# Performance work log

Hardware: AMD Instinct MI355X
Metric: run time of the kernel (lower is better)

## Reference

```python
import jax, jax.numpy as jnp
import numpy as np

E, D, H, B, S = 16, 1024, 256, 4, 4096  # num_splats, model_dim, ff_dim//num_splats, batch, seq_len


def setup_inputs() -> dict:
    key = jax.random.key(0)
    ks = jax.random.split(key, 8)
    s = 0.02  # init scale for stability
    return {
        "x": jax.random.normal(ks[0], (B, S, D), dtype=jnp.float32),
        "splat_id": jax.random.randint(ks[1], (S,), 0, E, dtype=jnp.int32),
        "W1": jax.random.normal(ks[2], (E, D, H), dtype=jnp.float32) * s,
        "b1": jnp.zeros((E, H), dtype=jnp.float32),
        "W2": jax.random.normal(ks[3], (E, H, D), dtype=jnp.float32) * s,
        "b2": jnp.zeros((E, D), dtype=jnp.float32),
        "Wg1": jax.random.normal(ks[4], (D, D), dtype=jnp.float32) * s,
        "bg1": jnp.zeros((D,), dtype=jnp.float32),
        "Wg2": jax.random.normal(ks[5], (D, D), dtype=jnp.float32) * s,
        "bg2": jnp.zeros((D,), dtype=jnp.float32),
    }


def reference(x, splat_id, W1, b1, W2, b2, Wg1, bg1, Wg2, bg2):
    # Splat-aware dispatch: token s is processed by expert splat_id[s].
    # Equivalent vectorized form: run every expert's small MLP, mask at the
    # hidden layer by expert assignment, and sum over experts (each token is
    # assigned to exactly one expert, matching the gather->MLP->scatter loop).
    nE = W1.shape[0]
    onehot = (splat_id[None, :] == jnp.arange(nE, dtype=splat_id.dtype)[:, None]).astype(x.dtype)  # [E,S]
    # hidden: [E,B,S,H]
    h = jax.nn.gelu(jnp.einsum('bsd,edh->ebsh', x, W1) + b1[:, None, None, :], approximate=False)
    h = h * onehot[:, None, :, None]  # zero tokens not routed to expert e
    routed = jnp.einsum('ebsh,ehd->bsd', h, W2)  # [B,S,D]
    routed = routed + jnp.einsum('es,ed->sd', onehot, b2)[None, :, :]  # per-token expert bias
    # global aggregator MLP (torch GELU default = exact erf form)
    g = jax.nn.gelu(routed @ Wg1 + bg1, approximate=False)
    return g @ Wg2 + bg2
```

## Files before the change

kernel.cpp:

```cpp
#include <hip/hip_runtime.h>


#define DEV __device__ __forceinline__

typedef float f32x4 __attribute__((ext_vector_type(4)));
typedef float f32x16 __attribute__((ext_vector_type(16)));
typedef short short8 __attribute__((ext_vector_type(8)));

DEV unsigned short f2bf(float f) {
  unsigned u = __float_as_uint(f);
  u += 0x7fffu + ((u >> 16) & 1u);
  return (unsigned short)(u >> 16);
}

DEV void gload_lds16(const void* g, void* l) {
  __builtin_amdgcn_global_load_lds(
      (const __attribute__((address_space(1))) unsigned int*)g,
      (__attribute__((address_space(3))) unsigned int*)l, 16, 0, 0);
}

DEV float gelu_exact(float v) {
  return 0.5f * v * (1.0f + erff(v * 0.70710678118654752f));
}

#define BARRIER() __builtin_amdgcn_s_barrier()
#define VMW(n)    asm volatile("s_waitcnt vmcnt(" #n ")" ::: "memory")

__global__ __launch_bounds__(256) void prep_kernel(
    const float* __restrict__ x, unsigned short* __restrict__ xb,
    const float* __restrict__ W1, unsigned short* __restrict__ w1t,
    const float* __restrict__ W2, unsigned short* __restrict__ w2t,
    const float* __restrict__ Wg1, unsigned short* __restrict__ wg1t,
    const float* __restrict__ Wg2, unsigned short* __restrict__ wg2t) {
  __shared__ float tile[64][65];
  const int t = threadIdx.x;
  int id = (int)blockIdx.x;
  if (id < 8192) {
    long i = ((long)id * 256 + t) * 8;
    float4 v0 = *(const float4*)(x + i);
    float4 v1 = *(const float4*)(x + i + 4);
    uint4 o;
    o.x = (unsigned)f2bf(v0.x) | ((unsigned)f2bf(v0.y) << 16);
    o.y = (unsigned)f2bf(v0.z) | ((unsigned)f2bf(v0.w) << 16);
    o.z = (unsigned)f2bf(v1.x) | ((unsigned)f2bf(v1.y) << 16);
    o.w = (unsigned)f2bf(v1.z) | ((unsigned)f2bf(v1.w) << 16);
    *(uint4*)(xb + i) = o;
    return;
  }
  id -= 8192;
  const float* in; unsigned short* out;
  int R, C, r0, c0; long base;
  if (id < 1024) {
    in = W1; out = w1t; R = 1024; C = 256;
    base = (long)(id >> 6) * 262144;
    r0 = ((id >> 2) & 15) * 64; c0 = (id & 3) * 64;
  } else if (id < 2048) {
    id -= 1024;
    in = W2; out = w2t; R = 256; C = 1024;
    base = (long)(id >> 6) * 262144;
    r0 = ((id >> 4) & 3) * 64; c0 = (id & 15) * 64;
  } else if (id < 2304) {
    id -= 2048;
    in = Wg1; out = wg1t; R = 1024; C = 1024; base = 0;
    r0 = (id >> 4) * 64; c0 = (id & 15) * 64;
  } else {
    id -= 2304;
    in = Wg2; out = wg2t; R = 1024; C = 1024; base = 0;
    r0 = (id >> 4) * 64; c0 = (id & 15) * 64;
  }
  const int cc = t & 63, rr = t >> 6;
#pragma unroll
  for (int i = 0; i < 16; i++) {
    int r = rr + i * 4;
    tile[r][cc] = in[base + (long)(r0 + r) * C + (c0 + cc)];
  }
  __syncthreads();
#pragma unroll
  for (int i = 0; i < 16; i++) {
    int c = rr + i * 4;
    out[base + (long)(c0 + c) * R + (r0 + cc)] = f2bf(tile[cc][c]);
  }
}

__global__ __launch_bounds__(256) void route_kernel(
    const int* __restrict__ sid, int S, int* __restrict__ offs, int* __restrict__ order,
    int* __restrict__ tileE, int* __restrict__ tileR, int* __restrict__ ntl) {
  __shared__ int cnt[16], cur[16];
  const int t = threadIdx.x;
  if (t < 16) cnt[t] = 0;
  __syncthreads();
  for (int s = t; s < S; s += 256) atomicAdd(&cnt[sid[s]], 1);
  __syncthreads();
  if (t == 0) {
    int a = 0;
    for (int e = 0; e < 16; e++) { offs[e] = a; cur[e] = a; a += cnt[e]; }
    offs[16] = a;
    int nt = 0;
    for (int e = 0; e < 16; e++) {
      const int rows = 4 * cnt[e];
      for (int r = 0; r < rows; r += 128) {
        tileE[nt] = e;
        tileR[nt] = 4 * offs[e] + r;
        nt++;
      }
    }
    ntl[0] = nt;
  }
  __syncthreads();
  for (int s = t; s < S; s += 256) {
    int p = atomicAdd(&cur[sid[s]], 1);
    order[p] = s;
  }
}

template <bool GATHER_A, bool SCATTER_C, bool GELU, bool OUT_F32>
__global__ __launch_bounds__(256) void gemm_mfma(
    const unsigned short* __restrict__ A, const unsigned short* __restrict__ BT,
    const float* __restrict__ bias, void* __restrict__ Cout,
    int N, int K,
    const int* __restrict__ order, const int* __restrict__ offs,
    const int* __restrict__ tileE, const int* __restrict__ tileR,
    const int* __restrict__ ntl,
    int S, long btStride, int biasStride) {
  const int ti = (int)blockIdx.y;
  if (ti >= ntl[0]) return;
  const int t = (int)threadIdx.x;
  const int lane = t & 63;
  const int w = t >> 6;
  const int wm = w >> 1, wn = w & 1;
  const int tileN = (int)blockIdx.x;

  const int e = tileE[ti];
  const int rowBase = tileR[ti];
  int Me = 4 * offs[e + 1] - rowBase;
  if (Me > 128) Me = 128;
  const unsigned short* bt = BT + (long)e * btStride;
  const float* bs = bias + (long)e * biasStride;

  __shared__ __align__(16) unsigned short lA[128 * 64];
  __shared__ __align__(16) unsigned short lB[128 * 64];

  const unsigned short* aSrc[4];
  const unsigned short* bSrc[4];
  {
    const int q = t & 7;
#pragma unroll
    for (int i = 0; i < 4; i++) {
      const int row = i * 32 + (t >> 3);
      const int koff = ((q * 16) ^ ((row & 7) << 4)) >> 1;
      const int rr = (row < Me) ? row : (Me - 1);
      const int g = rowBase + rr;
      long arow;
      if (GATHER_A) {
        const int s = order[g >> 2];
        arow = (long)(g & 3) * S + s;
      } else {
        arow = g;
      }
      aSrc[i] = A + arow * (long)K + koff;
      const int col = tileN * 128 + row;
      bSrc[i] = bt + (long)col * K + koff;
    }
  }

  f32x4 acc[4][4] = {};

  const int KT = K >> 6;
  for (int kt = 0; kt < KT; kt++) {
    __syncthreads();
#pragma unroll
    for (int i = 0; i < 4; i++) {
      gload_lds16(aSrc[i] + (kt << 6), (void*)(lA + i * 2048 + w * 512));
      gload_lds16(bSrc[i] + (kt << 6), (void*)(lB + i * 2048 + w * 512));
    }
    __syncthreads();
#pragma unroll
    for (int kk = 0; kk < 2; kk++) {
      short8 af[4], bfr[4];
      const int kbyte = kk * 64 + (lane >> 4) * 16;
#pragma unroll
      for (int mi = 0; mi < 4; mi++) {
        const int row = wm * 64 + mi * 16 + (lane & 15);
        const int off = row * 128 + (kbyte ^ ((row & 7) << 4));
        af[mi] = *(const short8*)((const char*)lA + off);
      }
#pragma unroll
      for (int ni = 0; ni < 4; ni++) {
        const int row = wn * 64 + ni * 16 + (lane & 15);
        const int off = row * 128 + (kbyte ^ ((row & 7) << 4));
        bfr[ni] = *(const short8*)((const char*)lB + off);
      }
#pragma unroll
      for (int mi = 0; mi < 4; mi++)
#pragma unroll
        for (int ni = 0; ni < 4; ni++)
          acc[mi][ni] = __builtin_amdgcn_mfma_f32_16x16x32_bf16(af[mi], bfr[ni], acc[mi][ni], 0, 0, 0);
    }
  }

  float bcol[4];
#pragma unroll
  for (int ni = 0; ni < 4; ni++)
    bcol[ni] = bs[tileN * 128 + wn * 64 + ni * 16 + (lane & 15)];

#pragma unroll
  for (int mi = 0; mi < 4; mi++) {
#pragma unroll
    for (int j = 0; j < 4; j++) {
      const int lrow = wm * 64 + mi * 16 + ((lane >> 4) * 4) + j;
      if (lrow >= Me) continue;
      const int g = rowBase + lrow;
      long crow;
      if (SCATTER_C) crow = (long)(g & 3) * S + order[g >> 2];
      else crow = g;
#pragma unroll
      for (int ni = 0; ni < 4; ni++) {
        float v = acc[mi][ni][j] + bcol[ni];
        if (GELU) v = gelu_exact(v);
        const long cidx = crow * (long)N + tileN * 128 + wn * 64 + ni * 16 + (lane & 15);
        if (OUT_F32) ((float*)Cout)[cidx] = v;
        else ((unsigned short*)Cout)[cidx] = f2bf(v);
      }
    }
  }
}

template <bool GELU, bool OUT_F32>
__global__ __launch_bounds__(512, 2) void gemm_8p32(
    const unsigned short* __restrict__ A, const unsigned short* __restrict__ BT,
    const float* __restrict__ bias, void* __restrict__ Cout,
    int N, int K, int ntiles) {
  __shared__ __align__(16) unsigned short lds[8 * 8192];

  const int t = (int)threadIdx.x;
  const int lane = t & 63;
  const int w = t >> 6;
  const int wm = w >> 2;
  const int wn = w & 3;

  const int cpx = (int)gridDim.x >> 3;
  const int swz = ((int)blockIdx.x & 7) * cpx + ((int)blockIdx.x >> 3);
  const int mtile = swz / ntiles, ntile = swz % ntiles;

  const int tq = t & 7;
  const unsigned short* srcA[2][2];
  const unsigned short* srcB[2][2];
#pragma unroll
  for (int i = 0; i < 2; i++) {
    const int ir = i * 64 + (t >> 3);
    const int koffE = ((tq * 16) ^ ((ir & 7) << 4)) >> 1;
#pragma unroll
    for (int h = 0; h < 2; h++) {
      const int ra = (ir & 63) + (h << 6) + ((ir >> 6) << 7);
      srcA[i][h] = A + (long)(mtile * 256 + ra) * K + koffE;
      const int cb = (ir & 31) + (h << 5) + ((ir >> 5) << 6);
      srcB[i][h] = BT + (long)(ntile * 256 + cb) * K + koffE;
    }
  }
  const int dstE = (t >> 3) * 64 + tq * 8;

  auto STAGE = [&](int d, int mat, int h, int kt) {
    unsigned short* dst = lds + ((d * 4 + mat * 2 + h) << 13) + dstE;
    const unsigned short* s0 = (mat == 0 ? srcA[0][h] : srcB[0][h]) + (kt << 6);
    const unsigned short* s1 = (mat == 0 ? srcA[1][h] : srcB[1][h]) + (kt << 6);
    gload_lds16(s0, dst);
    gload_lds16(s1, dst + 4096);
  };

  short8 aR[2][4], bR[2][4];
  const int kcol = ((lane >> 5) << 4);
  const int l31 = lane & 31;

  auto LDA = [&](int d, int mh) {
    const char* base = (const char*)(lds + ((d * 4 + mh) << 13));
    const int r0 = wm * 64 + l31;
#pragma unroll
    for (int m = 0; m < 2; m++) {
      const int row = r0 + m * 32;
      const int rs = (row & 7) << 4;
#pragma unroll
      for (int kk = 0; kk < 4; kk++)
        aR[m][kk] = *(const short8*)(base + row * 128 + ((kk * 32 + kcol) ^ rs));
    }
  };
  auto LDB = [&](int d, int nh) {
    const char* base = (const char*)(lds + ((d * 4 + 2 + nh) << 13));
    const int col = wn * 32 + l31;
    const int rs = (col & 7) << 4;
#pragma unroll
    for (int kk = 0; kk < 4; kk++)
      bR[nh][kk] = *(const short8*)(base + col * 128 + ((kk * 32 + kcol) ^ rs));
  };

  f32x16 acc[4][2] = {};
  auto MMA = [&](int mh, int nh) {
    __builtin_amdgcn_s_setprio(1);
#pragma unroll
    for (int kk = 0; kk < 4; kk++)
#pragma unroll
      for (int m = 0; m < 2; m++)
        acc[mh * 2 + m][nh] = __builtin_amdgcn_mfma_f32_32x32x16_bf16(
            aR[m][kk], bR[nh][kk], acc[mh * 2 + m][nh], 0, 0, 0);
    __builtin_amdgcn_s_setprio(0);
  };

  const int KT = K >> 6;

  {
    const int t1 = (KT > 1) ? 1 : 0;
    STAGE(0, 0, 0, 0); STAGE(0, 1, 0, 0); STAGE(0, 1, 1, 0); STAGE(0, 0, 1, 0);
    STAGE(1, 0, 0, t1); STAGE(1, 1, 0, t1); STAGE(1, 1, 1, t1);
    VMW(6);
    BARRIER();
  }

  for (int it = 0; it < (KT >> 1); ++it) {
    const int tb = (2 * it + 1 < KT) ? 2 * it + 1 : KT - 1;
    int nx = 2 * it + 2; if (nx >= KT) nx = KT - 1;
    int ny = 2 * it + 3; if (ny >= KT) ny = KT - 1;
    LDA(0, 0); LDB(0, 0); STAGE(1, 0, 1, tb);
    BARRIER();
    MMA(0, 0);
    BARRIER();
    LDB(0, 1); STAGE(0, 0, 0, nx);
    BARRIER();
    MMA(0, 1);
    BARRIER();
    LDA(0, 1); STAGE(0, 1, 0, nx);
    BARRIER();
    MMA(1, 0);
    BARRIER();
    STAGE(0, 1, 1, nx);
    BARRIER();
    MMA(1, 1);
    VMW(6);
    BARRIER();
    LDA(1, 0); LDB(1, 0); STAGE(0, 0, 1, nx);
    BARRIER();
    MMA(0, 0);
    BARRIER();
    LDB(1, 1); STAGE(1, 0, 0, ny);
    BARRIER();
    MMA(0, 1);
    BARRIER();
    LDA(1, 1); STAGE(1, 1, 0, ny);
    BARRIER();
    MMA(1, 0);
    BARRIER();
    STAGE(1, 1, 1, ny);
    BARRIER();
    MMA(1, 1);
    VMW(6);
    BARRIER();
  }
  VMW(0);

  float bc[2];
#pragma unroll
  for (int n = 0; n < 2; n++)
    bc[n] = bias[ntile * 256 + wn * 64 + n * 32 + l31];
  const int cbase = ntile * 256 + wn * 64 + l31;
  const int rbase = mtile * 256 + wm * 128 + ((lane >> 5) << 2);
#pragma unroll
  for (int mf = 0; mf < 4; mf++) {
#pragma unroll
    for (int reg = 0; reg < 16; reg++) {
      const long crow = rbase + mf * 32 + (reg & 3) + ((reg >> 2) << 3);
#pragma unroll
      for (int nf = 0; nf < 2; nf++) {
        float v = acc[mf][nf][reg] + bc[nf];
        if (GELU) v = gelu_exact(v);
        const long cidx = crow * (long)N + cbase + nf * 32;
        if (OUT_F32) ((float*)Cout)[cidx] = v;
        else ((unsigned short*)Cout)[cidx] = f2bf(v);
      }
    }
  }
}

extern "C" void kernel_launch(void* const* d_in, const int* in_sizes, int n_in,
                              void* d_out, int out_size, void* d_ws, size_t ws_size,
                              hipStream_t stream) {
  const float* x   = (const float*)d_in[0];
  const int*   sid = (const int*)d_in[1];
  const float* W1  = (const float*)d_in[2];
  const float* b1  = (const float*)d_in[3];
  const float* W2  = (const float*)d_in[4];
  const float* b2  = (const float*)d_in[5];
  const float* Wg1 = (const float*)d_in[6];
  const float* bg1 = (const float*)d_in[7];
  const float* Wg2 = (const float*)d_in[8];
  const float* bg2 = (const float*)d_in[9];
  (void)in_sizes; (void)n_in; (void)out_size; (void)ws_size;

  constexpr int D = 1024, H = 256, S = 4096, B = 4;
  constexpr long NT = (long)B * S;

  char* ws = (char*)d_ws;
  unsigned short* xb   = (unsigned short*)(ws);
  unsigned short* w1t  = (unsigned short*)(ws + 33554432);
  unsigned short* w2t  = (unsigned short*)(ws + 41943040);
  unsigned short* wg1t = (unsigned short*)(ws + 50331648);
  unsigned short* wg2t = (unsigned short*)(ws + 52428800);
  unsigned short* hbuf = (unsigned short*)(ws + 54525952);
  unsigned short* rout = (unsigned short*)(ws + 62914560);
  int* offs  = (int*)(ws + 96468992);
  int* order = (int*)(ws + 96469248);
  int* tileE = (int*)(ws + 96485632);
  int* tileR = (int*)(ws + 96486208);
  int* ntl   = (int*)(ws + 96486784);

  prep_kernel<<<dim3(10752), 256, 0, stream>>>(x, xb, W1, w1t, W2, w2t, Wg1, wg1t, Wg2, wg2t);
  route_kernel<<<1, 256, 0, stream>>>(sid, S, offs, order, tileE, tileR, ntl);

  gemm_mfma<true, false, true, false><<<dim3(H / 128, 144), 256, 0, stream>>>(
      xb, w1t, b1, hbuf, H, D, order, offs, tileE, tileR, ntl, S, (long)H * D, H);
  gemm_mfma<false, true, false, false><<<dim3(D / 128, 144), 256, 0, stream>>>(
      hbuf, w2t, b2, rout, D, H, order, offs, tileE, tileR, ntl, S, (long)D * H, D);
  gemm_8p32<true, false><<<dim3((unsigned)(NT / 256) * (D / 256)), 512, 0, stream>>>(
      rout, wg1t, bg1, xb, D, D, D / 256);
  gemm_8p32<false, true><<<dim3((unsigned)(NT / 256) * (D / 256)), 512, 0, stream>>>(
      xb, wg2t, bg2, d_out, D, D, D / 256);
}
```

Before: 194.6 us.

## Use 2-phase double-buffered GEMM for Wg1 and 16x16 MFMA in 8-phase kernel

Adds a new simple double-buffered GEMM (one stage load then a full 64-wide K compute per iteration, 16x16x32 MFMA, one block per CU) used for the first aggregator GEMM. The existing 8-phase kernel, kept for the second GEMM, is converted from 32x32x16 to 16x16x32 MFMA with a matching fragment layout and epilogue. The aim is to change the instruction mix and the synchronisation pattern of the aggregator GEMMs. The simpler kernel uses fewer barriers but gives up some load/compute overlap and occupancy.

```diff
diff --git a/kernel.cpp b/kernel.cpp
--- a/kernel.cpp
+++ b/kernel.cpp
@@ -4,7 +4,6 @@
 #define DEV __device__ __forceinline__
 
 typedef float f32x4 __attribute__((ext_vector_type(4)));
-typedef float f32x16 __attribute__((ext_vector_type(16)));
 typedef short short8 __attribute__((ext_vector_type(8)));
 
 DEV unsigned short f2bf(float f) {
@@ -13,7 +12,7 @@
   return (unsigned short)(u >> 16);
 }
 
-DEV void gload_lds16(const void* g, void* l) {
+DEV void gload16(const void* g, void* l) {
   __builtin_amdgcn_global_load_lds(
       (const __attribute__((address_space(1))) unsigned int*)g,
       (__attribute__((address_space(3))) unsigned int*)l, 16, 0, 0);
@@ -170,8 +169,8 @@
     __syncthreads();
 #pragma unroll
     for (int i = 0; i < 4; i++) {
-      gload_lds16(aSrc[i] + (kt << 6), (void*)(lA + i * 2048 + w * 512));
-      gload_lds16(bSrc[i] + (kt << 6), (void*)(lB + i * 2048 + w * 512));
+      gload16(aSrc[i] + (kt << 6), (void*)(lA + i * 2048 + w * 512));
+      gload16(bSrc[i] + (kt << 6), (void*)(lB + i * 2048 + w * 512));
     }
     __syncthreads();
 #pragma unroll
@@ -226,11 +225,11 @@
 }
 
 template <bool GELU, bool OUT_F32>
-__global__ __launch_bounds__(512, 2) void gemm_8p32(
+__global__ __launch_bounds__(512, 1) void gemm_2ph(
     const unsigned short* __restrict__ A, const unsigned short* __restrict__ BT,
     const float* __restrict__ bias, void* __restrict__ Cout,
     int N, int K, int ntiles) {
-  __shared__ __align__(16) unsigned short lds[8 * 8192];
+  __shared__ __align__(16) unsigned short lds[2][2][256 * 64];
 
   const int t = (int)threadIdx.x;
   const int lane = t & 63;
@@ -243,6 +242,100 @@
   const int mtile = swz / ntiles, ntile = swz % ntiles;
 
   const int tq = t & 7;
+  const unsigned short* srcA[4];
+  const unsigned short* srcB[4];
+#pragma unroll
+  for (int i = 0; i < 4; i++) {
+    const int row = i * 64 + (t >> 3);
+    const int koffE = ((tq * 16) ^ ((row & 7) << 4)) >> 1;
+    srcA[i] = A + (long)(mtile * 256 + row) * K + koffE;
+    srcB[i] = BT + (long)(ntile * 256 + row) * K + koffE;
+  }
+  const int dstE = (t >> 3) * 64 + tq * 8;
+
+  auto STAGE = [&](int buf, int kt) {
+    const long ko = (long)kt << 6;
+#pragma unroll
+    for (int i = 0; i < 4; i++) gload16(srcA[i] + ko, &lds[buf][0][i * 4096 + dstE]);
+#pragma unroll
+    for (int i = 0; i < 4; i++) gload16(srcB[i] + ko, &lds[buf][1][i * 4096 + dstE]);
+  };
+
+  f32x4 acc[8][4] = {};
+  const int KT = K >> 6;
+
+  STAGE(0, 0);
+  __syncthreads();
+
+  int buf = 0;
+  for (int kt = 0; kt < KT; kt++) {
+    if (kt + 1 < KT) STAGE(buf ^ 1, kt + 1);
+#pragma unroll
+    for (int kk = 0; kk < 2; kk++) {
+      short8 aF[8], bF[4];
+      const int kb = kk * 64 + ((lane >> 4) << 4);
+#pragma unroll
+      for (int m = 0; m < 8; m++) {
+        const int row = wm * 128 + m * 16 + (lane & 15);
+        aF[m] = *(const short8*)((const char*)&lds[buf][0][0] + row * 128 + (kb ^ ((row & 7) << 4)));
+      }
+#pragma unroll
+      for (int n = 0; n < 4; n++) {
+        const int row = wn * 64 + n * 16 + (lane & 15);
+        bF[n] = *(const short8*)((const char*)&lds[buf][1][0] + row * 128 + (kb ^ ((row & 7) << 4)));
+      }
+      __builtin_amdgcn_s_setprio(1);
+#pragma unroll
+      for (int m = 0; m < 8; m++)
+#pragma unroll
+        for (int n = 0; n < 4; n++)
+          acc[m][n] = __builtin_amdgcn_mfma_f32_16x16x32_bf16(aF[m], bF[n], acc[m][n], 0, 0, 0);
+      __builtin_amdgcn_s_setprio(0);
+    }
+    __syncthreads();
+    buf ^= 1;
+  }
+
+  float bcol[4];
+#pragma unroll
+  for (int n = 0; n < 4; n++)
+    bcol[n] = bias[ntile * 256 + wn * 64 + n * 16 + (lane & 15)];
+  const int cbase = ntile * 256 + wn * 64 + (lane & 15);
+#pragma unroll
+  for (int m = 0; m < 8; m++) {
+#pragma unroll
+    for (int j = 0; j < 4; j++) {
+      const long crow = mtile * 256 + wm * 128 + m * 16 + ((lane >> 4) << 2) + j;
+#pragma unroll
+      for (int n = 0; n < 4; n++) {
+        float v = acc[m][n][j] + bcol[n];
+        if (GELU) v = gelu_exact(v);
+        const long cidx = crow * (long)N + cbase + n * 16;
+        if (OUT_F32) ((float*)Cout)[cidx] = v;
+        else ((unsigned short*)Cout)[cidx] = f2bf(v);
+      }
+    }
+  }
+}
+
+template <bool GELU, bool OUT_F32>
+__global__ __launch_bounds__(512, 2) void gemm_8phase(
+    const unsigned short* __restrict__ A, const unsigned short* __restrict__ BT,
+    const float* __restrict__ bias, void* __restrict__ Cout,
+    int N, int K, int ntiles) {
+  __shared__ __align__(16) unsigned short lds[8 * 8192];
+
+  const int t = (int)threadIdx.x;
+  const int lane = t & 63;
+  const int w = t >> 6;
+  const int wm = w >> 2;
+  const int wn = w & 3;
+
+  const int cpx = (int)gridDim.x >> 3;
+  const int swz = ((int)blockIdx.x & 7) * cpx + ((int)blockIdx.x >> 3);
+  const int mtile = swz / ntiles, ntile = swz % ntiles;
+
+  const int tq = t & 7;
   const unsigned short* srcA[2][2];
   const unsigned short* srcB[2][2];
 #pragma unroll
@@ -263,44 +356,48 @@
     unsigned short* dst = lds + ((d * 4 + mat * 2 + h) << 13) + dstE;
     const unsigned short* s0 = (mat == 0 ? srcA[0][h] : srcB[0][h]) + (kt << 6);
     const unsigned short* s1 = (mat == 0 ? srcA[1][h] : srcB[1][h]) + (kt << 6);
-    gload_lds16(s0, dst);
-    gload_lds16(s1, dst + 4096);
+    gload16(s0, dst);
+    gload16(s1, dst + 4096);
   };
 
-  short8 aR[2][4], bR[2][4];
-  const int kcol = ((lane >> 5) << 4);
-  const int l31 = lane & 31;
+  short8 aReg[8], bReg[8];
+  const int klane = (lane >> 4) << 4;
+  const int rsw = (lane & 7) << 4;
 
   auto LDA = [&](int d, int mh) {
     const char* base = (const char*)(lds + ((d * 4 + mh) << 13));
-    const int r0 = wm * 64 + l31;
-#pragma unroll
-    for (int m = 0; m < 2; m++) {
-      const int row = r0 + m * 32;
-      const int rs = (row & 7) << 4;
-#pragma unroll
-      for (int kk = 0; kk < 4; kk++)
-        aR[m][kk] = *(const short8*)(base + row * 128 + ((kk * 32 + kcol) ^ rs));
+    const int r0 = wm * 64 + (lane & 15);
+#pragma unroll
+    for (int m = 0; m < 4; m++) {
+      const int row = r0 + m * 16;
+#pragma unroll
+      for (int kk = 0; kk < 2; kk++)
+        aReg[m * 2 + kk] = *(const short8*)(base + row * 128 + ((kk * 64 + klane) ^ rsw));
     }
   };
   auto LDB = [&](int d, int nh) {
     const char* base = (const char*)(lds + ((d * 4 + 2 + nh) << 13));
-    const int col = wn * 32 + l31;
-    const int rs = (col & 7) << 4;
-#pragma unroll
-    for (int kk = 0; kk < 4; kk++)
-      bR[nh][kk] = *(const short8*)(base + col * 128 + ((kk * 32 + kcol) ^ rs));
+    const int r0 = wn * 32 + (lane & 15);
+#pragma unroll
+    for (int n = 0; n < 2; n++) {
+      const int row = r0 + n * 16;
+#pragma unroll
+      for (int kk = 0; kk < 2; kk++)
+        bReg[(nh * 2 + n) * 2 + kk] = *(const short8*)(base + row * 128 + ((kk * 64 + klane) ^ rsw));
+    }
   };
 
-  f32x16 acc[4][2] = {};
-  auto MMA = [&](int mh, int nh) {
+  f32x4 acc[8][4] = {};
+  auto MMA = [&](int mb, int nb) {
     __builtin_amdgcn_s_setprio(1);
 #pragma unroll
-    for (int kk = 0; kk < 4; kk++)
-#pragma unroll
-      for (int m = 0; m < 2; m++)
-        acc[mh * 2 + m][nh] = __builtin_amdgcn_mfma_f32_32x32x16_bf16(
-            aR[m][kk], bR[nh][kk], acc[mh * 2 + m][nh], 0, 0, 0);
+    for (int kk = 0; kk < 2; kk++)
+#pragma unroll
+      for (int m = 0; m < 4; m++)
+#pragma unroll
+        for (int n = 0; n < 2; n++)
+          acc[mb + m][nb + n] = __builtin_amdgcn_mfma_f32_16x16x32_bf16(
+              aReg[m * 2 + kk], bReg[(nb + n) * 2 + kk], acc[mb + m][nb + n], 0, 0, 0);
     __builtin_amdgcn_s_setprio(0);
   };
 
@@ -324,15 +421,15 @@
     BARRIER();
     LDB(0, 1); STAGE(0, 0, 0, nx);
     BARRIER();
-    MMA(0, 1);
+    MMA(0, 2);
     BARRIER();
     LDA(0, 1); STAGE(0, 1, 0, nx);
     BARRIER();
-    MMA(1, 0);
+    MMA(4, 0);
     BARRIER();
     STAGE(0, 1, 1, nx);
     BARRIER();
-    MMA(1, 1);
+    MMA(4, 2);
     VMW(6);
     BARRIER();
     LDA(1, 0); LDB(1, 0); STAGE(0, 0, 1, nx);
@@ -341,36 +438,35 @@
     BARRIER();
     LDB(1, 1); STAGE(1, 0, 0, ny);
     BARRIER();
-    MMA(0, 1);
+    MMA(0, 2);
     BARRIER();
     LDA(1, 1); STAGE(1, 1, 0, ny);
     BARRIER();
-    MMA(1, 0);
+    MMA(4, 0);
     BARRIER();
     STAGE(1, 1, 1, ny);
     BARRIER();
-    MMA(1, 1);
+    MMA(4, 2);
     VMW(6);
     BARRIER();
   }
   VMW(0);
 
-  float bc[2];
-#pragma unroll
-  for (int n = 0; n < 2; n++)
-    bc[n] = bias[ntile * 256 + wn * 64 + n * 32 + l31];
-  const int cbase = ntile * 256 + wn * 64 + l31;
-  const int rbase = mtile * 256 + wm * 128 + ((lane >> 5) << 2);
-#pragma unroll
-  for (int mf = 0; mf < 4; mf++) {
-#pragma unroll
-    for (int reg = 0; reg < 16; reg++) {
-      const long crow = rbase + mf * 32 + (reg & 3) + ((reg >> 2) << 3);
-#pragma unroll
-      for (int nf = 0; nf < 2; nf++) {
-        float v = acc[mf][nf][reg] + bc[nf];
+  float bcol[4];
+#pragma unroll
+  for (int n = 0; n < 4; n++)
+    bcol[n] = bias[ntile * 256 + wn * 64 + n * 16 + (lane & 15)];
+  const int cbase = ntile * 256 + wn * 64 + (lane & 15);
+#pragma unroll
+  for (int m = 0; m < 8; m++) {
+#pragma unroll
+    for (int j = 0; j < 4; j++) {
+      const long crow = mtile * 256 + wm * 128 + m * 16 + ((lane >> 4) << 2) + j;
+#pragma unroll
+      for (int n = 0; n < 4; n++) {
+        float v = acc[m][n][j] + bcol[n];
         if (GELU) v = gelu_exact(v);
-        const long cidx = crow * (long)N + cbase + nf * 32;
+        const long cidx = crow * (long)N + cbase + n * 16;
         if (OUT_F32) ((float*)Cout)[cidx] = v;
         else ((unsigned short*)Cout)[cidx] = f2bf(v);
       }
@@ -417,8 +513,8 @@
       xb, w1t, b1, hbuf, H, D, order, offs, tileE, tileR, ntl, S, (long)H * D, H);
   gemm_mfma<false, true, false, false><<<dim3(D / 128, 144), 256, 0, stream>>>(
       hbuf, w2t, b2, rout, D, H, order, offs, tileE, tileR, ntl, S, (long)D * H, D);
-  gemm_8p32<true, false><<<dim3((unsigned)(NT / 256) * (D / 256)), 512, 0, stream>>>(
+  gemm_2ph<true, false><<<dim3((unsigned)(NT / 256) * (D / 256)), 512, 0, stream>>>(
       rout, wg1t, bg1, xb, D, D, D / 256);
-  gemm_8p32<false, true><<<dim3((unsigned)(NT / 256) * (D / 256)), 512, 0, stream>>>(
+  gemm_8phase<false, true><<<dim3((unsigned)(NT / 256) * (D / 256)), 512, 0, stream>>>(
       xb, wg2t, bg2, d_out, D, D, D / 256);
 }
```

Measured after the change: 186.5 us. 1.04x faster.

## Replace 256x256 ping-pong dense GEMM with simple 128x128 tile kernel

Applied to the files above, without the earlier changes.

The aggregator GEMMs move from a 512-thread, 256x256-tile kernel with a hand-scheduled double-buffered LDS pipeline and 32x32 MFMAs to a 256-thread, 128x128-tile kernel. The new kernel uses a single LDS buffer with two syncthreads per k-step and 16x16x32 MFMAs, the same scheme as the routed GEMM. This gives four times as many blocks and more occupancy per CU, but loses the overlap of loads with MFMA and the higher arithmetic intensity of the larger tiles.

```diff
diff --git a/kernel.cpp b/kernel.cpp
--- a/kernel.cpp
+++ b/kernel.cpp
@@ -4,7 +4,6 @@
 #define DEV __device__ __forceinline__
 
 typedef float f32x4 __attribute__((ext_vector_type(4)));
-typedef float f32x16 __attribute__((ext_vector_type(16)));
 typedef short short8 __attribute__((ext_vector_type(8)));
 
 DEV unsigned short f2bf(float f) {
@@ -13,7 +12,7 @@
   return (unsigned short)(u >> 16);
 }
 
-DEV void gload_lds16(const void* g, void* l) {
+DEV void gload16(const void* g, void* l) {
   __builtin_amdgcn_global_load_lds(
       (const __attribute__((address_space(1))) unsigned int*)g,
       (__attribute__((address_space(3))) unsigned int*)l, 16, 0, 0);
@@ -22,9 +21,6 @@
 DEV float gelu_exact(float v) {
   return 0.5f * v * (1.0f + erff(v * 0.70710678118654752f));
 }
-
-#define BARRIER() __builtin_amdgcn_s_barrier()
-#define VMW(n)    asm volatile("s_waitcnt vmcnt(" #n ")" ::: "memory")
 
 __global__ __launch_bounds__(256) void prep_kernel(
     const float* __restrict__ x, unsigned short* __restrict__ xb,
@@ -170,8 +166,8 @@
     __syncthreads();
 #pragma unroll
     for (int i = 0; i < 4; i++) {
-      gload_lds16(aSrc[i] + (kt << 6), (void*)(lA + i * 2048 + w * 512));
-      gload_lds16(bSrc[i] + (kt << 6), (void*)(lB + i * 2048 + w * 512));
+      gload16(aSrc[i] + (kt << 6), (void*)(lA + i * 2048 + w * 512));
+      gload16(bSrc[i] + (kt << 6), (void*)(lB + i * 2048 + w * 512));
     }
     __syncthreads();
 #pragma unroll
@@ -226,151 +222,85 @@
 }
 
 template <bool GELU, bool OUT_F32>
-__global__ __launch_bounds__(512, 2) void gemm_8p32(
+__global__ __launch_bounds__(256, 4) void gemm_dense128(
     const unsigned short* __restrict__ A, const unsigned short* __restrict__ BT,
     const float* __restrict__ bias, void* __restrict__ Cout,
     int N, int K, int ntiles) {
-  __shared__ __align__(16) unsigned short lds[8 * 8192];
-
   const int t = (int)threadIdx.x;
   const int lane = t & 63;
   const int w = t >> 6;
-  const int wm = w >> 2;
-  const int wn = w & 3;
+  const int wm = w >> 1, wn = w & 1;
 
   const int cpx = (int)gridDim.x >> 3;
   const int swz = ((int)blockIdx.x & 7) * cpx + ((int)blockIdx.x >> 3);
   const int mtile = swz / ntiles, ntile = swz % ntiles;
 
-  const int tq = t & 7;
-  const unsigned short* srcA[2][2];
-  const unsigned short* srcB[2][2];
-#pragma unroll
-  for (int i = 0; i < 2; i++) {
-    const int ir = i * 64 + (t >> 3);
-    const int koffE = ((tq * 16) ^ ((ir & 7) << 4)) >> 1;
-#pragma unroll
-    for (int h = 0; h < 2; h++) {
-      const int ra = (ir & 63) + (h << 6) + ((ir >> 6) << 7);
-      srcA[i][h] = A + (long)(mtile * 256 + ra) * K + koffE;
-      const int cb = (ir & 31) + (h << 5) + ((ir >> 5) << 6);
-      srcB[i][h] = BT + (long)(ntile * 256 + cb) * K + koffE;
-    }
-  }
-  const int dstE = (t >> 3) * 64 + tq * 8;
-
-  auto STAGE = [&](int d, int mat, int h, int kt) {
-    unsigned short* dst = lds + ((d * 4 + mat * 2 + h) << 13) + dstE;
-    const unsigned short* s0 = (mat == 0 ? srcA[0][h] : srcB[0][h]) + (kt << 6);
-    const unsigned short* s1 = (mat == 0 ? srcA[1][h] : srcB[1][h]) + (kt << 6);
-    gload_lds16(s0, dst);
-    gload_lds16(s1, dst + 4096);
-  };
-
-  short8 aR[2][4], bR[2][4];
-  const int kcol = ((lane >> 5) << 4);
-  const int l31 = lane & 31;
-
-  auto LDA = [&](int d, int mh) {
-    const char* base = (const char*)(lds + ((d * 4 + mh) << 13));
-    const int r0 = wm * 64 + l31;
-#pragma unroll
-    for (int m = 0; m < 2; m++) {
-      const int row = r0 + m * 32;
-      const int rs = (row & 7) << 4;
-#pragma unroll
-      for (int kk = 0; kk < 4; kk++)
-        aR[m][kk] = *(const short8*)(base + row * 128 + ((kk * 32 + kcol) ^ rs));
-    }
-  };
-  auto LDB = [&](int d, int nh) {
-    const char* base = (const char*)(lds + ((d * 4 + 2 + nh) << 13));
-    const int col = wn * 32 + l31;
-    const int rs = (col & 7) << 4;
-#pragma unroll
-    for (int kk = 0; kk < 4; kk++)
-      bR[nh][kk] = *(const short8*)(base + col * 128 + ((kk * 32 + kcol) ^ rs));
-  };
-
-  f32x16 acc[4][2] = {};
-  auto MMA = [&](int mh, int nh) {
-    __builtin_amdgcn_s_setprio(1);
-#pragma unroll
-    for (int kk = 0; kk < 4; kk++)
-#pragma unroll
-      for (int m = 0; m < 2; m++)
-        acc[mh * 2 + m][nh] = __builtin_amdgcn_mfma_f32_32x32x16_bf16(
-            aR[m][kk], bR[nh][kk], acc[mh * 2 + m][nh], 0, 0, 0);
-    __builtin_amdgcn_s_setprio(0);
-  };
+  __shared__ __align__(16) unsigned short lA[128 * 64];
+  __shared__ __align__(16) unsigned short lB[128 * 64];
+
+  const unsigned short* aSrc[4];
+  const unsigned short* bSrc[4];
+  {
+    const int q = t & 7;
+#pragma unroll
+    for (int i = 0; i < 4; i++) {
+      const int row = i * 32 + (t >> 3);
+      const int koff = ((q * 16) ^ ((row & 7) << 4)) >> 1;
+      aSrc[i] = A + (long)(mtile * 128 + row) * K + koff;
+      bSrc[i] = BT + (long)(ntile * 128 + row) * K + koff;
+    }
+  }
+
+  f32x4 acc[4][4] = {};
 
   const int KT = K >> 6;
-
-  {
-    const int t1 = (KT > 1) ? 1 : 0;
-    STAGE(0, 0, 0, 0); STAGE(0, 1, 0, 0); STAGE(0, 1, 1, 0); STAGE(0, 0, 1, 0);
-    STAGE(1, 0, 0, t1); STAGE(1, 1, 0, t1); STAGE(1, 1, 1, t1);
-    VMW(6);
-    BARRIER();
-  }
-
-  for (int it = 0; it < (KT >> 1); ++it) {
-    const int tb = (2 * it + 1 < KT) ? 2 * it + 1 : KT - 1;
-    int nx = 2 * it + 2; if (nx >= KT) nx = KT - 1;
-    int ny = 2 * it + 3; if (ny >= KT) ny = KT - 1;
-    LDA(0, 0); LDB(0, 0); STAGE(1, 0, 1, tb);
-    BARRIER();
-    MMA(0, 0);
-    BARRIER();
-    LDB(0, 1); STAGE(0, 0, 0, nx);
-    BARRIER();
-    MMA(0, 1);
-    BARRIER();
-    LDA(0, 1); STAGE(0, 1, 0, nx);
-    BARRIER();
-    MMA(1, 0);
-    BARRIER();
-    STAGE(0, 1, 1, nx);
-    BARRIER();
-    MMA(1, 1);
-    VMW(6);
-    BARRIER();
-    LDA(1, 0); LDB(1, 0); STAGE(0, 0, 1, nx);
-    BARRIER();
-    MMA(0, 0);
-    BARRIER();
-    LDB(1, 1); STAGE(1, 0, 0, ny);
-    BARRIER();
-    MMA(0, 1);
-    BARRIER();
-    LDA(1, 1); STAGE(1, 1, 0, ny);
-    BARRIER();
-    MMA(1, 0);
-    BARRIER();
-    STAGE(1, 1, 1, ny);
-    BARRIER();
-    MMA(1, 1);
-    VMW(6);
-    BARRIER();
-  }
-  VMW(0);
-
-  float bc[2];
-#pragma unroll
-  for (int n = 0; n < 2; n++)
-    bc[n] = bias[ntile * 256 + wn * 64 + n * 32 + l31];
-  const int cbase = ntile * 256 + wn * 64 + l31;
-  const int rbase = mtile * 256 + wm * 128 + ((lane >> 5) << 2);
-#pragma unroll
-  for (int mf = 0; mf < 4; mf++) {
-#pragma unroll
-    for (int reg = 0; reg < 16; reg++) {
-      const long crow = rbase + mf * 32 + (reg & 3) + ((reg >> 2) << 3);
-#pragma unroll
-      for (int nf = 0; nf < 2; nf++) {
-        float v = acc[mf][nf][reg] + bc[nf];
+  for (int kt = 0; kt < KT; kt++) {
+    __syncthreads();
+#pragma unroll
+    for (int i = 0; i < 4; i++) {
+      gload16(aSrc[i] + (kt << 6), (void*)(lA + i * 2048 + w * 512));
+      gload16(bSrc[i] + (kt << 6), (void*)(lB + i * 2048 + w * 512));
+    }
+    __syncthreads();
+#pragma unroll
+    for (int kk = 0; kk < 2; kk++) {
+      short8 af[4], bfr[4];
+      const int kbyte = kk * 64 + (lane >> 4) * 16;
+#pragma unroll
+      for (int mi = 0; mi < 4; mi++) {
+        const int row = wm * 64 + mi * 16 + (lane & 15);
+        const int off = row * 128 + (kbyte ^ ((row & 7) << 4));
+        af[mi] = *(const short8*)((const char*)lA + off);
+      }
+#pragma unroll
+      for (int ni = 0; ni < 4; ni++) {
+        const int row = wn * 64 + ni * 16 + (lane & 15);
+        const int off = row * 128 + (kbyte ^ ((row & 7) << 4));
+        bfr[ni] = *(const short8*)((const char*)lB + off);
+      }
+#pragma unroll
+      for (int mi = 0; mi < 4; mi++)
+#pragma unroll
+        for (int ni = 0; ni < 4; ni++)
+          acc[mi][ni] = __builtin_amdgcn_mfma_f32_16x16x32_bf16(af[mi], bfr[ni], acc[mi][ni], 0, 0, 0);
+    }
+  }
+
+  float bcol[4];
+#pragma unroll
+  for (int ni = 0; ni < 4; ni++)
+    bcol[ni] = bias[ntile * 128 + wn * 64 + ni * 16 + (lane & 15)];
+
+#pragma unroll
+  for (int mi = 0; mi < 4; mi++) {
+#pragma unroll
+    for (int j = 0; j < 4; j++) {
+      const long crow = mtile * 128 + wm * 64 + mi * 16 + ((lane >> 4) * 4) + j;
+#pragma unroll
+      for (int ni = 0; ni < 4; ni++) {
+        float v = acc[mi][ni][j] + bcol[ni];
         if (GELU) v = gelu_exact(v);
-        const long cidx = crow * (long)N + cbase + nf * 32;
+        const long cidx = crow * (long)N + ntile * 128 + wn * 64 + ni * 16 + (lane & 15);
         if (OUT_F32) ((float*)Cout)[cidx] = v;
         else ((unsigned short*)Cout)[cidx] = f2bf(v);
       }
@@ -417,8 +347,8 @@
       xb, w1t, b1, hbuf, H, D, order, offs, tileE, tileR, ntl, S, (long)H * D, H);
   gemm_mfma<false, true, false, false><<<dim3(D / 128, 144), 256, 0, stream>>>(
       hbuf, w2t, b2, rout, D, H, order, offs, tileE, tileR, ntl, S, (long)D * H, D);
-  gemm_8p32<true, false><<<dim3((unsigned)(NT / 256) * (D / 256)), 512, 0, stream>>>(
-      rout, wg1t, bg1, xb, D, D, D / 256);
-  gemm_8p32<false, true><<<dim3((unsigned)(NT / 256) * (D / 256)), 512, 0, stream>>>(
-      xb, wg2t, bg2, d_out, D, D, D / 256);
-}
+  gemm_dense128<true, false><<<dim3((unsigned)(NT / 128) * (D / 128)), 256, 0, stream>>>(
+      rout, wg1t, bg1, xb, D, D, D / 128);
+  gemm_dense128<false, true><<<dim3((unsigned)(NT / 128) * (D / 128)), 256, 0, stream>>>(
+      xb, wg2t, bg2, d_out, D, D, D / 128);
+}
```

New measurement: 182.8 us. 1.06x faster.
